# Kernel tuning notes

Hardware: AMD Instinct MI355X
Metric: run time of the kernel (lower is better)

Reference implementation:

```python
import jax, jax.numpy as jnp
import numpy as np


def setup_inputs() -> dict:
    key = jax.random.key(0)
    k1, k2, k3, k4 = jax.random.split(key, 4)
    N, F, E = 100000, 128, 1600000
    Fo = F // 2
    x = jax.random.normal(k1, (N, F), dtype=jnp.float32)
    edge_index = jax.random.randint(k2, (2, E), 0, N, dtype=jnp.int32)
    W_conv = jax.random.normal(k3, (Fo, F), dtype=jnp.float32) * (1.0 / np.sqrt(F))
    b_conv = jnp.zeros((Fo,), dtype=jnp.float32)
    W_lin = jax.random.normal(k4, (1, Fo), dtype=jnp.float32) * (1.0 / np.sqrt(Fo))
    b_lin = jnp.zeros((1,), dtype=jnp.float32)
    return {"x": x, "edge_index": edge_index, "W_conv": W_conv,
            "b_conv": b_conv, "W_lin": W_lin, "b_lin": b_lin}


def gcn_conv(x, edge_index, W_conv, b_conv):
    # PyG GCNConv: add self-loops, symmetric normalization, x@W.T, scatter-add, + bias
    N = x.shape[0]
    loops = jnp.arange(N, dtype=edge_index.dtype)
    src = jnp.concatenate([edge_index[0], loops])  # message sources
    dst = jnp.concatenate([edge_index[1], loops])  # aggregation targets
    h = x @ W_conv.T  # [N, Fo]
    deg = jax.ops.segment_sum(jnp.ones_like(dst, dtype=h.dtype), dst, num_segments=N)
    dinv = jnp.where(deg > 0, jax.lax.rsqrt(deg), 0.0)
    norm = dinv[src] * dinv[dst]  # [E+N]
    msg = h[src] * norm[:, None]  # [E+N, Fo] -- dominant memory traffic
    agg = jax.ops.segment_sum(msg, dst, num_segments=N)
    return agg + b_conv


def reference(x, edge_index, W_conv, b_conv, W_lin, b_lin):
    h = gcn_conv(x, edge_index, W_conv, b_conv)
    h = jax.nn.relu(h)
    logits = h @ W_lin.T + b_lin  # [N, 1]
    return jax.nn.sigmoid(logits)
```

## Files before the change

### kernel.cpp

```cpp
#include <hip/hip_runtime.h>
#include <hip/hip_bf16.h>
#include <math.h>

#define F_IN   128
#define F_OUT  64
#define CHUNK  5120
#define MAXB   512
#define PADSLACK 4096

typedef short bf16x8 __attribute__((ext_vector_type(8)));
typedef float f32x4  __attribute__((ext_vector_type(4)));
typedef float f32x2  __attribute__((ext_vector_type(2)));

__device__ __forceinline__ unsigned short f2bf(float f) {
    union { float f; unsigned int i; } c; c.f = f;
    unsigned int r = c.i + 0x7FFFu + ((c.i >> 16) & 1u);
    return (unsigned short)(r >> 16);
}
__device__ __forceinline__ unsigned int pk2bf(float a, float b) {
    __hip_bfloat162 p = __float22bfloat162_rn(make_float2(a, b));
    union { __hip_bfloat162 h; unsigned int u; } c; c.h = p; return c.u;
}
__device__ __forceinline__ float u_lo(unsigned int u) {
    union { unsigned int i; float f; } c; c.i = u << 16; return c.f;
}
__device__ __forceinline__ float u_hi(unsigned int u) {
    union { unsigned int i; float f; } c; c.i = u & 0xFFFF0000u; return c.f;
}

__global__ __launch_bounds__(256) void k_hist(
    const int* __restrict__ dst, int E, int* __restrict__ M, int NBLK, int NBC,
    const float* __restrict__ W, unsigned short* __restrict__ Wbf) {
    if (blockIdx.x == (unsigned)NBLK) {
        const float4* W4 = (const float4*)W;
        #pragma unroll
        for (int t = 0; t < 8; ++t) {
            int idx = t * 256 + threadIdx.x;
            float4 v = W4[idx];
            uint2 u = make_uint2(pk2bf(v.x, v.y), pk2bf(v.z, v.w));
            *(uint2*)&Wbf[idx * 4] = u;
        }
        return;
    }
    __shared__ int hist[MAXB];
    for (int c = threadIdx.x; c < MAXB; c += 256) hist[c] = 0;
    __syncthreads();
    int e0 = blockIdx.x * CHUNK;
    int e1 = min(E, e0 + CHUNK);
    for (int e = e0 + threadIdx.x; e < e1; e += 256)
        atomicAdd(&hist[dst[e] >> 8], 1);
    __syncthreads();
    for (int c = threadIdx.x; c < NBC; c += 256)
        M[c * NBLK + blockIdx.x] = hist[c];
}

__global__ void k_scan1(const int* __restrict__ M, int* __restrict__ tmp,
                        int* __restrict__ bsum, int S) {
    __shared__ int sh[256];
    int i = blockIdx.x * 256 + threadIdx.x;
    int v = (i < S) ? M[i] : 0;
    sh[threadIdx.x] = v;
    __syncthreads();
    for (int off = 1; off < 256; off <<= 1) {
        int t = (threadIdx.x >= off) ? sh[threadIdx.x - off] : 0;
        __syncthreads();
        sh[threadIdx.x] += t;
        __syncthreads();
    }
    if (i < S) tmp[i] = sh[threadIdx.x];
    if (threadIdx.x == 255) bsum[blockIdx.x] = sh[255];
}

__global__ void k_scan2(int* __restrict__ bsum, int NB1) {
    __shared__ int sh[512];
    int v = (threadIdx.x < NB1) ? bsum[threadIdx.x] : 0;
    sh[threadIdx.x] = v;
    __syncthreads();
    for (int off = 1; off < 512; off <<= 1) {
        int t = (threadIdx.x >= off) ? sh[threadIdx.x - off] : 0;
        __syncthreads();
        sh[threadIdx.x] += t;
        __syncthreads();
    }
    if (threadIdx.x < NB1) bsum[threadIdx.x] = sh[threadIdx.x] - v;
}

__device__ __forceinline__ int exscan(const int* M, const int* tmp, const int* bsum, int i) {
    return tmp[i] - M[i] + bsum[i >> 8];
}

__global__ __launch_bounds__(256) void k_scatter(
    const int* __restrict__ src, const int* __restrict__ dst, int E,
    const int* __restrict__ M, const int* __restrict__ tmp, const int* __restrict__ bsum,
    int NBLK, int NBC, unsigned int* __restrict__ entries) {
    __shared__ int cur[MAXB];
    for (int c = threadIdx.x; c < NBC; c += 256)
        cur[c] = exscan(M, tmp, bsum, c * NBLK + blockIdx.x);
    __syncthreads();
    int e0 = blockIdx.x * CHUNK;
    int e1 = min(E, e0 + CHUNK);
    for (int e = e0 + threadIdx.x; e < e1; e += 256) {
        int d = dst[e];
        int s = src[e];
        int p = atomicAdd(&cur[d >> 8], 1);
        entries[p] = ((unsigned int)(d & 255) << 24) | (unsigned int)s;
    }
}

__global__ __launch_bounds__(256) void k_sort(
    const unsigned int* __restrict__ entries,
    const int* __restrict__ M, const int* __restrict__ tmp, const int* __restrict__ bsum,
    int NBLK, int NBC, int E,
    int* __restrict__ offsetsP, int* __restrict__ deg,
    unsigned int* __restrict__ srcsP, int N) {
    __shared__ int hist[256];
    __shared__ int curs[256];
    __shared__ int sh_se[2];
    const int tid = threadIdx.x;
    const int b = blockIdx.x;
    if (tid == 0) {
        sh_se[0] = exscan(M, tmp, bsum, b * NBLK);
        sh_se[1] = (b + 1 < NBC) ? exscan(M, tmp, bsum, (b + 1) * NBLK) : E;
    }
    hist[tid] = 0;
    __syncthreads();
    const int start = sh_se[0];
    const int end   = sh_se[1];
    const int startP = start + b * PADSLACK;

    for (int i = start + tid; i < end; i += 256)
        atomicAdd(&hist[entries[i] >> 24], 1);
    __syncthreads();

    int cntv   = hist[tid];
    int padded = (cntv + 15) & ~15;
    curs[tid] = padded;
    __syncthreads();
    for (int off = 1; off < 256; off <<= 1) {
        int t = (tid >= off) ? curs[tid - off] : 0;
        __syncthreads();
        curs[tid] += t;
        __syncthreads();
    }
    int exclP = curs[tid] - padded;
    int d = (b << 8) + tid;
    if (d < N) { offsetsP[d] = startP + exclP; deg[d] = cntv; }
    __syncthreads();
    curs[tid] = startP + exclP;
    __syncthreads();

    for (int i = start + tid; i < end; i += 256) {
        unsigned int v = entries[i];
        int p = atomicAdd(&curs[v >> 24], 1);
        srcsP[p] = (v & 0xFFFFFFu) << 7;
    }
    __syncthreads();

    int padEnd = startP + exclP + padded;
    unsigned int sent = ((unsigned int)N) << 7;
    for (int p = curs[tid]; p < padEnd; ++p)
        srcsP[p] = sent;
}

__global__ __launch_bounds__(256) void k_gemm(
    const float* __restrict__ x, const unsigned short* __restrict__ Wbf,
    const int* __restrict__ deg, unsigned short* __restrict__ g, int N) {
    __shared__ unsigned short xs[64 * F_IN];
    __shared__ unsigned short Wsh[F_OUT * F_IN];
    __shared__ float dinvs[64];

    const int tid  = threadIdx.x;
    const int row0 = blockIdx.x * 64;

    {
        const uint2* Wb = (const uint2*)Wbf;
        #pragma unroll
        for (int t = 0; t < 8; ++t) {
            int idx = t * 256 + tid;
            *(uint2*)&Wsh[idx * 4] = Wb[idx];
        }
    }
    {
        const float4* x4 = (const float4*)x;
        #pragma unroll
        for (int t = 0; t < 8; ++t) {
            int idx = t * 256 + tid;
            int r = idx >> 5;
            int grow = row0 + r;
            float4 v = make_float4(0.f, 0.f, 0.f, 0.f);
            if (grow < N) v = x4[(size_t)grow * 32 + (idx & 31)];
            uint2 u = make_uint2(pk2bf(v.x, v.y), pk2bf(v.z, v.w));
            *(uint2*)&xs[idx * 4] = u;
        }
    }
    if (tid < 64) {
        int grow = row0 + tid;
        float dv = 1.0f;
        if (grow < N) dv = rsqrtf((float)deg[grow] + 1.0f);
        dinvs[tid] = dv;
    }
    __syncthreads();

    const int lane = tid & 63;
    const int wave = tid >> 6;
    const int m = lane & 15;
    const int q = lane >> 4;
    const int r0 = wave * 16;

    bf16x8 a[4];
    #pragma unroll
    for (int ks = 0; ks < 4; ++ks)
        a[ks] = *(const bf16x8*)&xs[(r0 + m) * F_IN + ks * 32 + q * 8];

    f32x4 acc[4] = {{0,0,0,0},{0,0,0,0},{0,0,0,0},{0,0,0,0}};
    #pragma unroll
    for (int ct = 0; ct < 4; ++ct) {
        #pragma unroll
        for (int ks = 0; ks < 4; ++ks) {
            bf16x8 b = *(const bf16x8*)&Wsh[(ct * 16 + m) * F_IN + ks * 32 + q * 8];
            acc[ct] = __builtin_amdgcn_mfma_f32_16x16x32_bf16(a[ks], b, acc[ct], 0, 0, 0);
        }
    }

    float dv[4];
    #pragma unroll
    for (int reg = 0; reg < 4; ++reg)
        dv[reg] = dinvs[r0 + q * 4 + reg];
    #pragma unroll
    for (int ct = 0; ct < 4; ++ct) {
        #pragma unroll
        for (int reg = 0; reg < 4; ++reg) {
            int grow = row0 + r0 + q * 4 + reg;
            if (grow <= N)
                g[(size_t)grow * F_OUT + ct * 16 + m] = f2bf(acc[ct][reg] * dv[reg]);
        }
    }
}

__global__ __launch_bounds__(256) void k_pull(
    const unsigned short* __restrict__ g, const int* __restrict__ offsetsP,
    const int* __restrict__ deg, const unsigned int* __restrict__ srcsP,
    const float* __restrict__ b_conv, const float* __restrict__ W_lin,
    const float* __restrict__ b_lin, float* __restrict__ out, int N) {
    const int lane   = threadIdx.x & 63;
    const int grp    = lane >> 3;
    const int s      = lane & 7;
    const int wave   = (blockIdx.x * blockDim.x + threadIdx.x) >> 6;
    const int nwaves = (gridDim.x * blockDim.x) >> 6;

    const float2* b2 = (const float2*)b_conv;
    const float2* w2 = (const float2*)W_lin;
    f32x2 bb[4], wl[4];
    #pragma unroll
    for (int j = 0; j < 4; ++j) {
        float2 tb = b2[s * 4 + j]; bb[j] = (f32x2){tb.x, tb.y};
        float2 tw = w2[s * 4 + j]; wl[j] = (f32x2){tw.x, tw.y};
    }
    const float bl = b_lin[0];
    const float selfm = (grp == 0) ? 1.0f : 0.0f;
    const f32x2 selfv = (f32x2){selfm, selfm};

    const char* gb = (const char*)g;
    const unsigned int seg = ((unsigned int)s) << 4;

    for (int i = wave; i < N; i += nwaves) {
        int e0 = __builtin_amdgcn_readfirstlane(offsetsP[i]);
        int dg = __builtin_amdgcn_readfirstlane(deg[i]);
        int niter = (dg + 15) >> 4;

        uint4 us = *(const uint4*)(gb + (size_t)(((unsigned int)i << 7) | seg));
        f32x2 acc[4];
        acc[0] = selfv * (f32x2){u_lo(us.x), u_hi(us.x)};
        acc[1] = selfv * (f32x2){u_lo(us.y), u_hi(us.y)};
        acc[2] = selfv * (f32x2){u_lo(us.z), u_hi(us.z)};
        acc[3] = selfv * (f32x2){u_lo(us.w), u_hi(us.w)};

        const unsigned int* sp = srcsP + e0;
        for (int it = 0; it < niter; ++it) {
            unsigned int o0 = sp[grp];
            unsigned int o1 = sp[8 + grp];
            uint4 uA = *(const uint4*)(gb + (size_t)(o0 | seg));
            uint4 uB = *(const uint4*)(gb + (size_t)(o1 | seg));
            acc[0] += (f32x2){u_lo(uA.x), u_hi(uA.x)};
            acc[1] += (f32x2){u_lo(uA.y), u_hi(uA.y)};
            acc[2] += (f32x2){u_lo(uA.z), u_hi(uA.z)};
            acc[3] += (f32x2){u_lo(uA.w), u_hi(uA.w)};
            acc[0] += (f32x2){u_lo(uB.x), u_hi(uB.x)};
            acc[1] += (f32x2){u_lo(uB.y), u_hi(uB.y)};
            acc[2] += (f32x2){u_lo(uB.z), u_hi(uB.z)};
            acc[3] += (f32x2){u_lo(uB.w), u_hi(uB.w)};
            sp += 16;
        }

        #pragma unroll
        for (int m = 8; m <= 32; m <<= 1) {
            #pragma unroll
            for (int j = 0; j < 4; ++j) {
                f32x2 t = (f32x2){__shfl_xor(acc[j][0], m, 64),
                                  __shfl_xor(acc[j][1], m, 64)};
                acc[j] += t;
            }
        }

        float dinv = rsqrtf((float)dg + 1.0f);
        f32x2 dinv2 = (f32x2){dinv, dinv};
        f32x2 dot2 = (f32x2){0.f, 0.f};
        #pragma unroll
        for (int j = 0; j < 4; ++j) {
            f32x2 r = acc[j] * dinv2 + bb[j];
            r[0] = fmaxf(r[0], 0.f);
            r[1] = fmaxf(r[1], 0.f);
            dot2 += r * wl[j];
        }
        float t = dot2[0] + dot2[1];
        t += __shfl_xor(t, 1, 64);
        t += __shfl_xor(t, 2, 64);
        t += __shfl_xor(t, 4, 64);
        if (lane == 0)
            out[i] = 1.0f / (1.0f + expf(-(t + bl)));
    }
}

extern "C" void kernel_launch(void* const* d_in, const int* in_sizes, int n_in,
                              void* d_out, int out_size, void* d_ws, size_t ws_size,
                              hipStream_t stream) {
    const float* x      = (const float*)d_in[0];
    const int*   ei     = (const int*)d_in[1];
    const float* W_conv = (const float*)d_in[2];
    const float* b_conv = (const float*)d_in[3];
    const float* W_lin  = (const float*)d_in[4];
    const float* b_lin  = (const float*)d_in[5];

    const int N = in_sizes[0] / F_IN;
    const int E = in_sizes[1] / 2;
    const int* src = ei;
    const int* dst = ei + E;
    float* out = (float*)d_out;

    const int NBC  = (N + 255) >> 8;
    const int NBLK = (E + CHUNK - 1) / CHUNK;
    const int S    = NBC * NBLK;
    const int NB1  = (S + 255) / 256;

    const int Na = (N + 256) & ~255;
    const int Sa = (S + 256) & ~255;
    const int Ea = (E + 255) & ~255;
    const int EPa = (E + NBC * PADSLACK + 511) & ~255;

    int* M         = (int*)d_ws;
    int* tmp       = M + Sa;
    int* bsum      = tmp + Sa;
    int* offsetsP  = bsum + 512;
    int* deg       = offsetsP + Na;
    unsigned short* Wbf = (unsigned short*)(deg + Na);
    unsigned int* entries = (unsigned int*)(Wbf + 8192);
    unsigned int* srcsP   = entries + Ea;
    unsigned short* g = (unsigned short*)(srcsP + EPa);

    k_hist   <<<NBLK + 1, 256, 0, stream>>>(dst, E, M, NBLK, NBC, W_conv, Wbf);
    k_scan1  <<<NB1, 256, 0, stream>>>(M, tmp, bsum, S);
    k_scan2  <<<1, 512, 0, stream>>>(bsum, NB1);
    k_scatter<<<NBLK, 256, 0, stream>>>(src, dst, E, M, tmp, bsum, NBLK, NBC, entries);
    k_sort   <<<NBC, 256, 0, stream>>>(entries, M, tmp, bsum, NBLK, NBC, E,
                                       offsetsP, deg, srcsP, N);
    k_gemm   <<<(N + 64) / 64, 256, 0, stream>>>(x, Wbf, deg, g, N);
    k_pull   <<<4096, 256, 0, stream>>>(g, offsetsP, deg, srcsP, b_conv, W_lin, b_lin, out, N);
}
```

Measured before the change: 194.6 us.

## Fuse partition kernels into one cooperative kernel with grid syncs

Replaces the five separate partitioning kernels (histogram, two scan passes, scatter, per-bucket sort) with a single cooperative kernel of 512 blocks that loops over chunks and separates the phases with grid.sync. It targets per-launch overhead and the idle gaps between small kernels. The cost is that each phase now runs on a fixed grid, and the sort phase has about 391 buckets for 512 blocks. Grid-wide barriers also carry their own latency, and the single-block scan becomes a serial point while the other blocks wait.

```diff
diff --git a/kernel.cpp b/kernel.cpp
--- a/kernel.cpp
+++ b/kernel.cpp
@@ -1,12 +1,16 @@
 #include <hip/hip_runtime.h>
 #include <hip/hip_bf16.h>
+#include <hip/hip_cooperative_groups.h>
 #include <math.h>
+
+namespace cg = cooperative_groups;
 
 #define F_IN   128
 #define F_OUT  64
 #define CHUNK  5120
 #define MAXB   512
 #define PADSLACK 4096
+#define PART_GRID 512
 
 typedef short bf16x8 __attribute__((ext_vector_type(8)));
 typedef float f32x4  __attribute__((ext_vector_type(4)));
@@ -28,138 +32,148 @@
     union { unsigned int i; float f; } c; c.i = u & 0xFFFF0000u; return c.f;
 }
 
-__global__ __launch_bounds__(256) void k_hist(
-    const int* __restrict__ dst, int E, int* __restrict__ M, int NBLK, int NBC,
-    const float* __restrict__ W, unsigned short* __restrict__ Wbf) {
-    if (blockIdx.x == (unsigned)NBLK) {
-        const float4* W4 = (const float4*)W;
-        #pragma unroll
-        for (int t = 0; t < 8; ++t) {
-            int idx = t * 256 + threadIdx.x;
-            float4 v = W4[idx];
-            uint2 u = make_uint2(pk2bf(v.x, v.y), pk2bf(v.z, v.w));
-            *(uint2*)&Wbf[idx * 4] = u;
-        }
-        return;
-    }
-    __shared__ int hist[MAXB];
-    for (int c = threadIdx.x; c < MAXB; c += 256) hist[c] = 0;
-    __syncthreads();
-    int e0 = blockIdx.x * CHUNK;
-    int e1 = min(E, e0 + CHUNK);
-    for (int e = e0 + threadIdx.x; e < e1; e += 256)
-        atomicAdd(&hist[dst[e] >> 8], 1);
-    __syncthreads();
-    for (int c = threadIdx.x; c < NBC; c += 256)
-        M[c * NBLK + blockIdx.x] = hist[c];
-}
-
-__global__ void k_scan1(const int* __restrict__ M, int* __restrict__ tmp,
-                        int* __restrict__ bsum, int S) {
-    __shared__ int sh[256];
-    int i = blockIdx.x * 256 + threadIdx.x;
-    int v = (i < S) ? M[i] : 0;
-    sh[threadIdx.x] = v;
-    __syncthreads();
-    for (int off = 1; off < 256; off <<= 1) {
-        int t = (threadIdx.x >= off) ? sh[threadIdx.x - off] : 0;
-        __syncthreads();
-        sh[threadIdx.x] += t;
-        __syncthreads();
-    }
-    if (i < S) tmp[i] = sh[threadIdx.x];
-    if (threadIdx.x == 255) bsum[blockIdx.x] = sh[255];
-}
-
-__global__ void k_scan2(int* __restrict__ bsum, int NB1) {
-    __shared__ int sh[512];
-    int v = (threadIdx.x < NB1) ? bsum[threadIdx.x] : 0;
-    sh[threadIdx.x] = v;
-    __syncthreads();
-    for (int off = 1; off < 512; off <<= 1) {
-        int t = (threadIdx.x >= off) ? sh[threadIdx.x - off] : 0;
-        __syncthreads();
-        sh[threadIdx.x] += t;
-        __syncthreads();
-    }
-    if (threadIdx.x < NB1) bsum[threadIdx.x] = sh[threadIdx.x] - v;
-}
+union PartShared {
+    int hist[MAXB];
+    int scan[512];
+    struct { int hist[256]; int curs[256]; int se[2]; } sort;
+};
 
 __device__ __forceinline__ int exscan(const int* M, const int* tmp, const int* bsum, int i) {
     return tmp[i] - M[i] + bsum[i >> 8];
 }
 
-__global__ __launch_bounds__(256) void k_scatter(
+__global__ __launch_bounds__(256, 8) void k_part(
     const int* __restrict__ src, const int* __restrict__ dst, int E,
-    const int* __restrict__ M, const int* __restrict__ tmp, const int* __restrict__ bsum,
-    int NBLK, int NBC, unsigned int* __restrict__ entries) {
-    __shared__ int cur[MAXB];
-    for (int c = threadIdx.x; c < NBC; c += 256)
-        cur[c] = exscan(M, tmp, bsum, c * NBLK + blockIdx.x);
-    __syncthreads();
-    int e0 = blockIdx.x * CHUNK;
-    int e1 = min(E, e0 + CHUNK);
-    for (int e = e0 + threadIdx.x; e < e1; e += 256) {
-        int d = dst[e];
-        int s = src[e];
-        int p = atomicAdd(&cur[d >> 8], 1);
-        entries[p] = ((unsigned int)(d & 255) << 24) | (unsigned int)s;
-    }
-}
-
-__global__ __launch_bounds__(256) void k_sort(
-    const unsigned int* __restrict__ entries,
-    const int* __restrict__ M, const int* __restrict__ tmp, const int* __restrict__ bsum,
-    int NBLK, int NBC, int E,
+    int* __restrict__ M, int* __restrict__ tmp, int* __restrict__ bsum,
     int* __restrict__ offsetsP, int* __restrict__ deg,
-    unsigned int* __restrict__ srcsP, int N) {
-    __shared__ int hist[256];
-    __shared__ int curs[256];
-    __shared__ int sh_se[2];
+    unsigned int* __restrict__ entries, unsigned int* __restrict__ srcsP,
+    int N, int NBC, int NCH, int S, int NB1,
+    const float* __restrict__ W, unsigned short* __restrict__ Wbf) {
+    cg::grid_group grid = cg::this_grid();
+    __shared__ PartShared su;
     const int tid = threadIdx.x;
-    const int b = blockIdx.x;
-    if (tid == 0) {
-        sh_se[0] = exscan(M, tmp, bsum, b * NBLK);
-        sh_se[1] = (b + 1 < NBC) ? exscan(M, tmp, bsum, (b + 1) * NBLK) : E;
-    }
-    hist[tid] = 0;
-    __syncthreads();
-    const int start = sh_se[0];
-    const int end   = sh_se[1];
-    const int startP = start + b * PADSLACK;
-
-    for (int i = start + tid; i < end; i += 256)
-        atomicAdd(&hist[entries[i] >> 24], 1);
-    __syncthreads();
-
-    int cntv   = hist[tid];
-    int padded = (cntv + 15) & ~15;
-    curs[tid] = padded;
-    __syncthreads();
-    for (int off = 1; off < 256; off <<= 1) {
-        int t = (tid >= off) ? curs[tid - off] : 0;
-        __syncthreads();
-        curs[tid] += t;
-        __syncthreads();
-    }
-    int exclP = curs[tid] - padded;
-    int d = (b << 8) + tid;
-    if (d < N) { offsetsP[d] = startP + exclP; deg[d] = cntv; }
-    __syncthreads();
-    curs[tid] = startP + exclP;
-    __syncthreads();
-
-    for (int i = start + tid; i < end; i += 256) {
-        unsigned int v = entries[i];
-        int p = atomicAdd(&curs[v >> 24], 1);
-        srcsP[p] = (v & 0xFFFFFFu) << 7;
-    }
-    __syncthreads();
-
-    int padEnd = startP + exclP + padded;
-    unsigned int sent = ((unsigned int)N) << 7;
-    for (int p = curs[tid]; p < padEnd; ++p)
-        srcsP[p] = sent;
+    const int G = gridDim.x;
+
+    if (blockIdx.x < 8) {
+        int idx = blockIdx.x * 256 + tid;
+        float4 v = ((const float4*)W)[idx];
+        uint2 u = make_uint2(pk2bf(v.x, v.y), pk2bf(v.z, v.w));
+        *(uint2*)&Wbf[idx * 4] = u;
+    }
+
+    for (int c = blockIdx.x; c < NCH; c += G) {
+        for (int k = tid; k < MAXB; k += 256) su.hist[k] = 0;
+        __syncthreads();
+        int e0 = c * CHUNK, e1 = min(E, e0 + CHUNK);
+        for (int e = e0 + tid; e < e1; e += 256)
+            atomicAdd(&su.hist[dst[e] >> 8], 1);
+        __syncthreads();
+        for (int k = tid; k < NBC; k += 256)
+            M[k * NCH + c] = su.hist[k];
+        __syncthreads();
+    }
+    __threadfence();
+    grid.sync();
+
+    for (int grp = blockIdx.x; grp < NB1; grp += G) {
+        int i = grp * 256 + tid;
+        int v = (i < S) ? M[i] : 0;
+        su.scan[tid] = v;
+        __syncthreads();
+        for (int off = 1; off < 256; off <<= 1) {
+            int t = (tid >= off) ? su.scan[tid - off] : 0;
+            __syncthreads();
+            su.scan[tid] += t;
+            __syncthreads();
+        }
+        if (i < S) tmp[i] = su.scan[tid];
+        if (tid == 255) bsum[grp] = su.scan[255];
+        __syncthreads();
+    }
+    __threadfence();
+    grid.sync();
+
+    if (blockIdx.x == 0) {
+        int v0 = (tid < NB1) ? bsum[tid] : 0;
+        int v1 = (256 + tid < NB1) ? bsum[256 + tid] : 0;
+        su.scan[tid] = v0;
+        su.scan[256 + tid] = v1;
+        __syncthreads();
+        for (int off = 1; off < 512; off <<= 1) {
+            int a = (tid >= off) ? su.scan[tid - off] : 0;
+            int b = (256 + tid >= off) ? su.scan[256 + tid - off] : 0;
+            __syncthreads();
+            su.scan[tid] += a;
+            su.scan[256 + tid] += b;
+            __syncthreads();
+        }
+        if (tid < NB1) bsum[tid] = su.scan[tid] - v0;
+        if (256 + tid < NB1) bsum[256 + tid] = su.scan[256 + tid] - v1;
+    }
+    __threadfence();
+    grid.sync();
+
+    for (int c = blockIdx.x; c < NCH; c += G) {
+        for (int k = tid; k < NBC; k += 256)
+            su.hist[k] = exscan(M, tmp, bsum, k * NCH + c);
+        __syncthreads();
+        int e0 = c * CHUNK, e1 = min(E, e0 + CHUNK);
+        for (int e = e0 + tid; e < e1; e += 256) {
+            int d = dst[e];
+            int s = src[e];
+            int p = atomicAdd(&su.hist[d >> 8], 1);
+            entries[p] = ((unsigned int)(d & 255) << 24) | (unsigned int)s;
+        }
+        __syncthreads();
+    }
+    __threadfence();
+    grid.sync();
+
+    for (int b = blockIdx.x; b < NBC; b += G) {
+        if (tid == 0) {
+            su.sort.se[0] = exscan(M, tmp, bsum, b * NCH);
+            su.sort.se[1] = (b + 1 < NBC) ? exscan(M, tmp, bsum, (b + 1) * NCH) : E;
+        }
+        su.sort.hist[tid] = 0;
+        __syncthreads();
+        const int start = su.sort.se[0];
+        const int end   = su.sort.se[1];
+        const int startP = start + b * PADSLACK;
+
+        for (int i = start + tid; i < end; i += 256)
+            atomicAdd(&su.sort.hist[entries[i] >> 24], 1);
+        __syncthreads();
+
+        int cntv   = su.sort.hist[tid];
+        int padded = (cntv + 15) & ~15;
+        su.sort.curs[tid] = padded;
+        __syncthreads();
+        for (int off = 1; off < 256; off <<= 1) {
+            int t = (tid >= off) ? su.sort.curs[tid - off] : 0;
+            __syncthreads();
+            su.sort.curs[tid] += t;
+            __syncthreads();
+        }
+        int exclP = su.sort.curs[tid] - padded;
+        int d = (b << 8) + tid;
+        if (d < N) { offsetsP[d] = startP + exclP; deg[d] = cntv; }
+        __syncthreads();
+        su.sort.curs[tid] = startP + exclP;
+        __syncthreads();
+
+        for (int i = start + tid; i < end; i += 256) {
+            unsigned int v = entries[i];
+            int p = atomicAdd(&su.sort.curs[v >> 24], 1);
+            srcsP[p] = (v & 0xFFFFFFu) << 7;
+        }
+        __syncthreads();
+
+        int padEnd = startP + exclP + padded;
+        unsigned int sent = ((unsigned int)N) << 7;
+        for (int p = su.sort.curs[tid]; p < padEnd; ++p)
+            srcsP[p] = sent;
+        __syncthreads();
+    }
 }
 
 __global__ __launch_bounds__(256) void k_gemm(
@@ -337,10 +351,10 @@
     const int* dst = ei + E;
     float* out = (float*)d_out;
 
-    const int NBC  = (N + 255) >> 8;
-    const int NBLK = (E + CHUNK - 1) / CHUNK;
-    const int S    = NBC * NBLK;
-    const int NB1  = (S + 255) / 256;
+    const int NBC = (N + 255) >> 8;
+    const int NCH = (E + CHUNK - 1) / CHUNK;
+    const int S   = NBC * NCH;
+    const int NB1 = (S + 255) / 256;
 
     const int Na = (N + 256) & ~255;
     const int Sa = (S + 256) & ~255;
@@ -357,12 +371,16 @@
     unsigned int* srcsP   = entries + Ea;
     unsigned short* g = (unsigned short*)(srcsP + EPa);
 
-    k_hist   <<<NBLK + 1, 256, 0, stream>>>(dst, E, M, NBLK, NBC, W_conv, Wbf);
-    k_scan1  <<<NB1, 256, 0, stream>>>(M, tmp, bsum, S);
-    k_scan2  <<<1, 512, 0, stream>>>(bsum, NB1);
-    k_scatter<<<NBLK, 256, 0, stream>>>(src, dst, E, M, tmp, bsum, NBLK, NBC, entries);
-    k_sort   <<<NBC, 256, 0, stream>>>(entries, M, tmp, bsum, NBLK, NBC, E,
-                                       offsetsP, deg, srcsP, N);
-    k_gemm   <<<(N + 64) / 64, 256, 0, stream>>>(x, Wbf, deg, g, N);
-    k_pull   <<<4096, 256, 0, stream>>>(g, offsetsP, deg, srcsP, b_conv, W_lin, b_lin, out, N);
-}
+    int E_ = E, N_ = N, NBC_ = NBC, NCH_ = NCH, S_ = S, NB1_ = NB1;
+    void* args[] = { (void*)&src, (void*)&dst, (void*)&E_,
+                     (void*)&M, (void*)&tmp, (void*)&bsum,
+                     (void*)&offsetsP, (void*)&deg,
+                     (void*)&entries, (void*)&srcsP,
+                     (void*)&N_, (void*)&NBC_, (void*)&NCH_, (void*)&S_, (void*)&NB1_,
+                     (void*)&W_conv, (void*)&Wbf };
+    hipLaunchCooperativeKernel((const void*)k_part, dim3(PART_GRID), dim3(256),
+                               args, 0, stream);
+
+    k_gemm<<<(N + 64) / 64, 256, 0, stream>>>(x, Wbf, deg, g, N);
+    k_pull<<<4096, 256, 0, stream>>>(g, offsetsP, deg, srcsP, b_conv, W_lin, b_lin, out, N);
+}
```

After: 616.2 us. 217% more time.
